# Kernel tuning notes

Measured on AMD Instinct MI355X. Metric: run time of the kernel, lower is better.

Reference implementation:

```python
import jax, jax.numpy as jnp
import numpy as np

LAMBDA = 10.0
BETA = 10.0
W = 5  # window size per axis (5,5,5); padding=2 hardcoded in original
DN = ('NCDHW', 'OIDHW', 'NCDHW')


def box_mean(x):
    """Uniform 5x5x5 box-filter mean with zero padding=2, via separable 1D convs."""
    specs = [((1, 1, W, 1, 1), [(2, 2), (0, 0), (0, 0)]),
             ((1, 1, 1, W, 1), [(0, 0), (2, 2), (0, 0)]),
             ((1, 1, 1, 1, W), [(0, 0), (0, 0), (2, 2)])]
    for kshape, pads in specs:
        k = jnp.full(kshape, 1.0 / W, dtype=x.dtype)
        x = jax.lax.conv_general_dilated(x, k, (1, 1, 1), pads, dimension_numbers=DN)
    return x


def lcc_loss(gt, pred):
    omega = gt.size
    d_gt = gt - box_mean(gt)
    d_pred = pred - box_mean(pred)
    num = jnp.square(jnp.sum(d_gt * d_pred))
    den = jnp.sum(jnp.square(d_gt)) * jnp.sum(jnp.square(d_pred))
    den = jnp.maximum(den, 1e-5)
    return -(1.0 / omega) * (num / den)


def reg_field_loss(reg_gt, reg_pred):
    omega = reg_gt.size
    return jnp.sqrt(jnp.sum(jnp.square(reg_pred - reg_gt))) / omega


def tversky_loss2(seg_gt, seg_pred):
    den = jnp.maximum(jnp.sum(seg_gt + seg_pred), 1e-5)
    return -0.5 * jnp.sum(2.0 * seg_gt * seg_pred) / den


def setup_inputs() -> dict:
    key = jax.random.key(0)
    ks = jax.random.split(key, 10)
    shp_f = (2, 3, 128, 128, 128)
    shp_i = (2, 1, 128, 128, 128)
    return {
        'F_0': jax.random.normal(ks[0], shp_f, jnp.float32),
        'F_0g': jax.random.normal(ks[1], shp_f, jnp.float32),
        'I_0': jax.random.uniform(ks[2], shp_i, jnp.float32),
        'I_0R': jax.random.uniform(ks[3], shp_i, jnp.float32),
        'I_1': jax.random.uniform(ks[4], shp_i, jnp.float32),
        'I_1R': jax.random.uniform(ks[5], shp_i, jnp.float32),
        'S_0': jax.random.uniform(ks[6], shp_i, jnp.float32),
        'S_0g': jax.random.uniform(ks[7], shp_i, jnp.float32),
        'S_1': jax.random.uniform(ks[8], shp_i, jnp.float32),
        'S_1g': jax.random.uniform(ks[9], shp_i, jnp.float32),
    }


def reference(F_0, F_0g, I_0, I_0R, I_1, I_1R, S_0, S_0g, S_1, S_1g):
    return (reg_field_loss(F_0, F_0g)
            + LAMBDA * (lcc_loss(I_0, I_0R) + lcc_loss(I_1, I_1R))
            + BETA * (tversky_loss2(S_0, S_0g) + tversky_loss2(S_1, S_1g)))
```

## Files before the change

kernel.cpp:

```cpp
#include <hip/hip_runtime.h>
#include <math.h>

#define VOL   (128*128*128)
#define PLANE (128*128)

#define LCC_BLOCKS   512
#define SQ_BLOCKS    1024
#define TV_BLOCKS    512
#define TOTAL_BLOCKS 2048


__device__ __forceinline__ double wave_reduce_d(double v) {
    #pragma unroll
    for (int off = 32; off > 0; off >>= 1)
        v += __shfl_down(v, off, 64);
    return v;
}

__device__ __forceinline__ void block_reduce1_atomic(double a, double* dst) {
    __shared__ double s1[4];
    int lane = threadIdx.x & 63;
    int wave = threadIdx.x >> 6;
    a = wave_reduce_d(a);
    if (lane == 0) s1[wave] = a;
    __syncthreads();
    if (threadIdx.x == 0)
        atomicAdd(&dst[0], s1[0] + s1[1] + s1[2] + s1[3]);
}

__device__ __forceinline__ void block_reduce2_atomic(double a, double b, double* dst) {
    __shared__ double s2[2][4];
    int lane = threadIdx.x & 63;
    int wave = threadIdx.x >> 6;
    a = wave_reduce_d(a);
    b = wave_reduce_d(b);
    if (lane == 0) { s2[0][wave] = a; s2[1][wave] = b; }
    __syncthreads();
    if (threadIdx.x == 0) {
        atomicAdd(&dst[0], s2[0][0] + s2[0][1] + s2[0][2] + s2[0][3]);
        atomicAdd(&dst[1], s2[1][0] + s2[1][1] + s2[1][2] + s2[1][3]);
    }
}

__device__ __forceinline__ void block_reduce3_atomic(double a, double b, double c, double* dst) {
    __shared__ double s3[3][4];
    int lane = threadIdx.x & 63;
    int wave = threadIdx.x >> 6;
    a = wave_reduce_d(a);
    b = wave_reduce_d(b);
    c = wave_reduce_d(c);
    if (lane == 0) { s3[0][wave] = a; s3[1][wave] = b; s3[2][wave] = c; }
    __syncthreads();
    if (threadIdx.x == 0) {
        atomicAdd(&dst[0], s3[0][0] + s3[0][1] + s3[0][2] + s3[0][3]);
        atomicAdd(&dst[1], s3[1][0] + s3[1][1] + s3[1][2] + s3[1][3]);
        atomicAdd(&dst[2], s3[2][0] + s3[2][1] + s3[2][2] + s3[2][3]);
    }
}


__global__ void zero_ws_kernel(double* ws) {
    if (threadIdx.x < 16) ws[threadIdx.x] = 0.0;
}


__global__ __launch_bounds__(256) void mega_kernel(
    const float* __restrict__ F0,  const float* __restrict__ F0g,
    const float* __restrict__ I0,  const float* __restrict__ I0R,
    const float* __restrict__ I1,  const float* __restrict__ I1R,
    const float* __restrict__ S0,  const float* __restrict__ S0g,
    const float* __restrict__ S1,  const float* __restrict__ S1g,
    double* __restrict__ ws)
{
    int b = blockIdx.x;
    int tid = threadIdx.x;
    int r = b & 3;

    if (r == 0) {
        __shared__ float xrow[4][2][4][68];

        int lb = b >> 2;
        int w  = tid >> 6;
        int l  = tid & 63;
        int wid = lb * 4 + w;
        int pair  = wid >> 10;
        int batch = (wid >> 9) & 1;
        int zs    = (wid >> 6) & 7;
        int yt    = (wid >> 1) & 31;
        int xt    = wid & 1;
        int x0 = xt << 6, y0 = yt << 2, z0 = zs << 4;

        const float* Vg = (pair ? I1  : I0)  + (size_t)batch * VOL;
        const float* Vp = (pair ? I1R : I0R) + (size_t)batch * VOL;
        double* dst = ws + (pair ? 4 : 1);

        int x  = x0 + l;
        int hx = x0 + ((l < 2) ? (l - 2) : (62 + l));
        int hxc = hx < 0 ? 0 : (hx > 127 ? 127 : hx);
        bool hok = (hx >= 0) && (hx < 128);
        int hslot = (l < 2) ? l : (64 + l);

        float (*rowg)[68] = xrow[w][0];
        float (*rowp)[68] = xrow[w][1];

        float psg[5][4], psp[5][4];
        float cg1[4] = {0,0,0,0}, cg2[4] = {0,0,0,0};
        float cp1[4] = {0,0,0,0}, cp2[4] = {0,0,0,0};
        float a1 = 0.f, a2 = 0.f, a3 = 0.f;

        for (int o = 0; o < 4; ++o) {
            #pragma unroll
            for (int u = 0; u < 5; ++u) {
                int it = o * 5 + u;
                int zp = z0 - 2 + it;
                bool zok = (zp >= 0) && (zp < 128);
                int zpc = zp < 0 ? 0 : (zp > 127 ? 127 : zp);
                size_t zoff = (size_t)zpc * PLANE;

                float vg[8], vp[8], hg[8], hp[8];
                #pragma unroll
                for (int j = 0; j < 8; ++j) {
                    int gy = y0 - 2 + j;
                    bool ok = zok && (gy >= 0) && (gy < 128);
                    int gyc = gy < 0 ? 0 : (gy > 127 ? 127 : gy);
                    size_t ro = zoff + (size_t)gyc * 128;
                    float tg = Vg[ro + x];
                    float tp = Vp[ro + x];
                    vg[j] = ok ? tg : 0.0f;
                    vp[j] = ok ? tp : 0.0f;
                    float thg = 0.0f, thp = 0.0f;
                    if (l < 4) { thg = Vg[ro + hxc]; thp = Vp[ro + hxc]; }
                    hg[j] = (ok && hok) ? thg : 0.0f;
                    hp[j] = (ok && hok) ? thp : 0.0f;
                }
                #pragma unroll
                for (int k = 0; k < 4; ++k) {
                    rowg[k][2 + l] = vg[k] + vg[k+1] + vg[k+2] + vg[k+3] + vg[k+4];
                    rowp[k][2 + l] = vp[k] + vp[k+1] + vp[k+2] + vp[k+3] + vp[k+4];
                }
                if (l < 4) {
                    #pragma unroll
                    for (int k = 0; k < 4; ++k) {
                        rowg[k][hslot] = hg[k] + hg[k+1] + hg[k+2] + hg[k+3] + hg[k+4];
                        rowp[k][hslot] = hp[k] + hp[k+1] + hp[k+2] + hp[k+3] + hp[k+4];
                    }
                }
                #pragma unroll
                for (int k = 0; k < 4; ++k) {
                    psg[u][k] = rowg[k][l] + rowg[k][l+1] + rowg[k][l+2]
                              + rowg[k][l+3] + rowg[k][l+4];
                    psp[u][k] = rowp[k][l] + rowp[k][l+1] + rowp[k][l+2]
                              + rowp[k][l+3] + rowp[k][l+4];
                }
                if (it >= 4) {
                    #pragma unroll
                    for (int k = 0; k < 4; ++k) {
                        float mg = (psg[0][k] + psg[1][k] + psg[2][k] + psg[3][k] + psg[4][k])
                                   * (1.0f / 125.0f);
                        float mp = (psp[0][k] + psp[1][k] + psp[2][k] + psp[3][k] + psp[4][k])
                                   * (1.0f / 125.0f);
                        float dg = cg2[k] - mg;
                        float dp = cp2[k] - mp;
                        a1 += dg * dp;
                        a2 += dg * dg;
                        a3 += dp * dp;
                    }
                }
                #pragma unroll
                for (int k = 0; k < 4; ++k) {
                    cg2[k] = cg1[k]; cg1[k] = vg[k + 2];
                    cp2[k] = cp1[k]; cp1[k] = vp[k + 2];
                }
            }
        }
        block_reduce3_atomic((double)a1, (double)a2, (double)a3, dst);

    } else if (r != 3) {
        int bid = (b >> 2) * 2 + (r - 1);
        const float4* A = (const float4*)F0;
        const float4* B = (const float4*)F0g;
        int idx = bid * 256 + tid;
        const int stride = SQ_BLOCKS * 256;
        float acc = 0.f;
        #pragma unroll
        for (int k = 0; k < 12; ++k) {
            int i = idx + k * stride;
            float4 xx = A[i], yy = B[i];
            float d0 = yy.x - xx.x, d1 = yy.y - xx.y;
            float d2 = yy.z - xx.z, d3 = yy.w - xx.w;
            acc += (d0 * d0 + d1 * d1) + (d2 * d2 + d3 * d3);
        }
        block_reduce1_atomic((double)acc, &ws[0]);

    } else {
        int idx0 = b >> 2;
        int pair = idx0 >> 8;
        int bid  = idx0 & 255;
        const float4* Gp = (const float4*)(pair ? S1 : S0);
        const float4* Pp = (const float4*)(pair ? S1g : S0g);
        double* dst = ws + (pair ? 9 : 7);
        int idx = bid * 256 + tid;
        const int stride = 256 * 256;
        float asum = 0.f, aprod = 0.f;
        #pragma unroll
        for (int k = 0; k < 16; ++k) {
            int i = idx + k * stride;
            float4 xx = Gp[i], yy = Pp[i];
            asum  += (xx.x + yy.x) + (xx.y + yy.y) + (xx.z + yy.z) + (xx.w + yy.w);
            aprod += (xx.x * yy.x + xx.y * yy.y) + (xx.z * yy.z + xx.w * yy.w);
        }
        block_reduce2_atomic((double)asum, (double)aprod, dst);
    }
}

__global__ void finalize_kernel(const double* __restrict__ ws, float* out) {
    if (threadIdx.x == 0 && blockIdx.x == 0) {
        double reg = sqrt(ws[0]) / 12582912.0;

        double num0 = ws[1] * ws[1];
        double den0 = ws[2] * ws[3];
        if (den0 < 1e-5) den0 = 1e-5;
        double l0 = -(1.0 / 4194304.0) * (num0 / den0);

        double num1 = ws[4] * ws[4];
        double den1 = ws[5] * ws[6];
        if (den1 < 1e-5) den1 = 1e-5;
        double l1 = -(1.0 / 4194304.0) * (num1 / den1);

        double td0 = ws[7]; if (td0 < 1e-5) td0 = 1e-5;
        double t0 = -ws[8] / td0;
        double td1 = ws[9]; if (td1 < 1e-5) td1 = 1e-5;
        double t1 = -ws[10] / td1;

        out[0] = (float)(reg + 10.0 * (l0 + l1) + 10.0 * (t0 + t1));
    }
}


extern "C" void kernel_launch(void* const* d_in, const int* in_sizes, int n_in,
                              void* d_out, int out_size, void* d_ws, size_t ws_size,
                              hipStream_t stream) {
    double* ws = (double*)d_ws;
    float* out = (float*)d_out;

    const float* F0  = (const float*)d_in[0];
    const float* F0g = (const float*)d_in[1];
    const float* I0  = (const float*)d_in[2];
    const float* I0R = (const float*)d_in[3];
    const float* I1  = (const float*)d_in[4];
    const float* I1R = (const float*)d_in[5];
    const float* S0  = (const float*)d_in[6];
    const float* S0g = (const float*)d_in[7];
    const float* S1  = (const float*)d_in[8];
    const float* S1g = (const float*)d_in[9];

    zero_ws_kernel<<<1, 64, 0, stream>>>(ws);
    mega_kernel<<<TOTAL_BLOCKS, 256, 0, stream>>>(F0, F0g, I0, I0R, I1, I1R,
                                                  S0, S0g, S1, S1g, ws);
    finalize_kernel<<<1, 64, 0, stream>>>(ws, out);
}
```

Measured before the change: 312.5 us.

## Restructure LCC box filter with float4 rows, shuffle x-sums and shared y-sums

New measurement: 280.9 us. -10.1%, faster.

```diff
diff --git a/kernel.cpp b/kernel.cpp
--- a/kernel.cpp
+++ b/kernel.cpp
@@ -4,9 +4,7 @@
 #define VOL   (128*128*128)
 #define PLANE (128*128)
 
-#define LCC_BLOCKS   512
 #define SQ_BLOCKS    1024
-#define TV_BLOCKS    512
 #define TOTAL_BLOCKS 2048
 
 
@@ -63,6 +61,22 @@
     if (threadIdx.x < 16) ws[threadIdx.x] = 0.0;
 }
 
+__device__ __forceinline__ float4 xbox(float4 b, int q) {
+    float lz = __shfl_up(b.z, 1, 32);
+    float lw = __shfl_up(b.w, 1, 32);
+    float rx = __shfl_down(b.x, 1, 32);
+    float ry = __shfl_down(b.y, 1, 32);
+    if (q == 0)  { lz = 0.0f; lw = 0.0f; }
+    if (q == 31) { rx = 0.0f; ry = 0.0f; }
+    float s = b.x + b.y + b.z + b.w;
+    float4 o;
+    o.x = lz + lw + (s - b.w);
+    o.y = lw + s;
+    o.z = s + rx;
+    o.w = (s - b.x) + rx + ry;
+    return o;
+}
+
 
 __global__ __launch_bounds__(256) void mega_kernel(
     const float* __restrict__ F0,  const float* __restrict__ F0g,
@@ -77,99 +91,94 @@
     int r = b & 3;
 
     if (r == 0) {
-        __shared__ float xrow[4][2][4][68];
+        __shared__ float4 xbuf[2][2][12][32];
 
         int lb = b >> 2;
-        int w  = tid >> 6;
-        int l  = tid & 63;
-        int wid = lb * 4 + w;
-        int pair  = wid >> 10;
-        int batch = (wid >> 9) & 1;
-        int zs    = (wid >> 6) & 7;
-        int yt    = (wid >> 1) & 31;
-        int xt    = wid & 1;
-        int x0 = xt << 6, y0 = yt << 2, z0 = zs << 4;
+        int q  = tid & 31;
+        int rg = tid >> 5;
+        int yt = lb & 15, zs = (lb >> 4) & 7;
+        int batch = (lb >> 7) & 1, pair = lb >> 8;
+        int y0 = yt << 3, z0 = zs << 4;
 
         const float* Vg = (pair ? I1  : I0)  + (size_t)batch * VOL;
         const float* Vp = (pair ? I1R : I0R) + (size_t)batch * VOL;
         double* dst = ws + (pair ? 4 : 1);
 
-        int x  = x0 + l;
-        int hx = x0 + ((l < 2) ? (l - 2) : (62 + l));
-        int hxc = hx < 0 ? 0 : (hx > 127 ? 127 : hx);
-        bool hok = (hx >= 0) && (hx < 128);
-        int hslot = (l < 2) ? l : (64 + l);
-
-        float (*rowg)[68] = xrow[w][0];
-        float (*rowp)[68] = xrow[w][1];
-
-        float psg[5][4], psp[5][4];
-        float cg1[4] = {0,0,0,0}, cg2[4] = {0,0,0,0};
-        float cp1[4] = {0,0,0,0}, cp2[4] = {0,0,0,0};
+        int ry1 = y0 - 2 + rg;
+        int ry2 = y0 + 6 + rg;
+        bool ok1 = (ry1 >= 0);
+        bool ok2 = (rg < 4) && (ry2 < 128);
+        int ry1c = ok1 ? ry1 : 0;
+        int ry2c = (ry2 < 128) ? ry2 : 0;
+
+        float4 ringg[5], ringp[5];
         float a1 = 0.f, a2 = 0.f, a3 = 0.f;
 
         for (int o = 0; o < 4; ++o) {
             #pragma unroll
             for (int u = 0; u < 5; ++u) {
                 int it = o * 5 + u;
-                int zp = z0 - 2 + it;
-                bool zok = (zp >= 0) && (zp < 128);
-                int zpc = zp < 0 ? 0 : (zp > 127 ? 127 : zp);
-                size_t zoff = (size_t)zpc * PLANE;
-
-                float vg[8], vp[8], hg[8], hp[8];
+                int z  = z0 - 2 + it;
+                bool zok = (z >= 0) && (z < 128);
+                int zc = zok ? z : 0;
+                size_t zb = (size_t)zc * PLANE;
+                int par = it & 1;
+
+                float4 g1 = ((const float4*)(Vg + zb + (size_t)ry1c * 128))[q];
+                float4 p1 = ((const float4*)(Vp + zb + (size_t)ry1c * 128))[q];
+                float4 g2 = make_float4(0.f,0.f,0.f,0.f), p2 = g2;
+                if (rg < 4) {
+                    g2 = ((const float4*)(Vg + zb + (size_t)ry2c * 128))[q];
+                    p2 = ((const float4*)(Vp + zb + (size_t)ry2c * 128))[q];
+                }
+                float4 cg = make_float4(0.f,0.f,0.f,0.f), cp = cg;
+                if (it >= 4) {
+                    size_t co = (size_t)(z - 2) * PLANE + (size_t)(y0 + rg) * 128;
+                    cg = ((const float4*)(Vg + co))[q];
+                    cp = ((const float4*)(Vp + co))[q];
+                }
+
+                bool v1 = zok && ok1, v2 = zok && ok2;
+                if (!v1) { g1 = make_float4(0.f,0.f,0.f,0.f); p1 = g1; }
+                if (!v2) { g2 = make_float4(0.f,0.f,0.f,0.f); p2 = g2; }
+
+                xbuf[par][0][rg][q] = xbox(g1, q);
+                xbuf[par][1][rg][q] = xbox(p1, q);
+                if (rg < 4) {
+                    xbuf[par][0][8 + rg][q] = xbox(g2, q);
+                    xbuf[par][1][8 + rg][q] = xbox(p2, q);
+                }
+                __syncthreads();
+
+                float4 yg = make_float4(0.f,0.f,0.f,0.f), yp = yg;
                 #pragma unroll
-                for (int j = 0; j < 8; ++j) {
-                    int gy = y0 - 2 + j;
-                    bool ok = zok && (gy >= 0) && (gy < 128);
-                    int gyc = gy < 0 ? 0 : (gy > 127 ? 127 : gy);
-                    size_t ro = zoff + (size_t)gyc * 128;
-                    float tg = Vg[ro + x];
-                    float tp = Vp[ro + x];
-                    vg[j] = ok ? tg : 0.0f;
-                    vp[j] = ok ? tp : 0.0f;
-                    float thg = 0.0f, thp = 0.0f;
-                    if (l < 4) { thg = Vg[ro + hxc]; thp = Vp[ro + hxc]; }
-                    hg[j] = (ok && hok) ? thg : 0.0f;
-                    hp[j] = (ok && hok) ? thp : 0.0f;
-                }
-                #pragma unroll
-                for (int k = 0; k < 4; ++k) {
-                    rowg[k][2 + l] = vg[k] + vg[k+1] + vg[k+2] + vg[k+3] + vg[k+4];
-                    rowp[k][2 + l] = vp[k] + vp[k+1] + vp[k+2] + vp[k+3] + vp[k+4];
-                }
-                if (l < 4) {
-                    #pragma unroll
-                    for (int k = 0; k < 4; ++k) {
-                        rowg[k][hslot] = hg[k] + hg[k+1] + hg[k+2] + hg[k+3] + hg[k+4];
-                        rowp[k][hslot] = hp[k] + hp[k+1] + hp[k+2] + hp[k+3] + hp[k+4];
-                    }
-                }
-                #pragma unroll
-                for (int k = 0; k < 4; ++k) {
-                    psg[u][k] = rowg[k][l] + rowg[k][l+1] + rowg[k][l+2]
-                              + rowg[k][l+3] + rowg[k][l+4];
-                    psp[u][k] = rowp[k][l] + rowp[k][l+1] + rowp[k][l+2]
-                              + rowp[k][l+3] + rowp[k][l+4];
-                }
+                for (int j = 0; j < 5; ++j) {
+                    float4 tg = xbuf[par][0][rg + j][q];
+                    float4 tp = xbuf[par][1][rg + j][q];
+                    yg.x += tg.x; yg.y += tg.y; yg.z += tg.z; yg.w += tg.w;
+                    yp.x += tp.x; yp.y += tp.y; yp.z += tp.z; yp.w += tp.w;
+                }
+                ringg[u] = yg;
+                ringp[u] = yp;
+
                 if (it >= 4) {
-                    #pragma unroll
-                    for (int k = 0; k < 4; ++k) {
-                        float mg = (psg[0][k] + psg[1][k] + psg[2][k] + psg[3][k] + psg[4][k])
-                                   * (1.0f / 125.0f);
-                        float mp = (psp[0][k] + psp[1][k] + psp[2][k] + psp[3][k] + psp[4][k])
-                                   * (1.0f / 125.0f);
-                        float dg = cg2[k] - mg;
-                        float dp = cp2[k] - mp;
-                        a1 += dg * dp;
-                        a2 += dg * dg;
-                        a3 += dp * dp;
-                    }
-                }
-                #pragma unroll
-                for (int k = 0; k < 4; ++k) {
-                    cg2[k] = cg1[k]; cg1[k] = vg[k + 2];
-                    cp2[k] = cp1[k]; cp1[k] = vp[k + 2];
+                    const float inv = 1.0f / 125.0f;
+                    float4 mg, mp;
+                    mg.x = (ringg[0].x+ringg[1].x+ringg[2].x+ringg[3].x+ringg[4].x)*inv;
+                    mg.y = (ringg[0].y+ringg[1].y+ringg[2].y+ringg[3].y+ringg[4].y)*inv;
+                    mg.z = (ringg[0].z+ringg[1].z+ringg[2].z+ringg[3].z+ringg[4].z)*inv;
+                    mg.w = (ringg[0].w+ringg[1].w+ringg[2].w+ringg[3].w+ringg[4].w)*inv;
+                    mp.x = (ringp[0].x+ringp[1].x+ringp[2].x+ringp[3].x+ringp[4].x)*inv;
+                    mp.y = (ringp[0].y+ringp[1].y+ringp[2].y+ringp[3].y+ringp[4].y)*inv;
+                    mp.z = (ringp[0].z+ringp[1].z+ringp[2].z+ringp[3].z+ringp[4].z)*inv;
+                    mp.w = (ringp[0].w+ringp[1].w+ringp[2].w+ringp[3].w+ringp[4].w)*inv;
+                    float dgx = cg.x - mg.x, dgy = cg.y - mg.y;
+                    float dgz = cg.z - mg.z, dgw = cg.w - mg.w;
+                    float dpx = cp.x - mp.x, dpy = cp.y - mp.y;
+                    float dpz = cp.z - mp.z, dpw = cp.w - mp.w;
+                    a1 += dgx*dpx + dgy*dpy + dgz*dpz + dgw*dpw;
+                    a2 += dgx*dgx + dgy*dgy + dgz*dgz + dgw*dgw;
+                    a3 += dpx*dpx + dpy*dpy + dpz*dpz + dpw*dpw;
                 }
             }
         }
```
